# Kernel tuning notes

Hardware: AMD Instinct MI355X
Metric: run time of the kernel (lower is better)

Reference implementation:

```python
import jax, jax.numpy as jnp
import numpy as np

DIM = 256
DH = 32
HEADS = DIM // DH
AG = 6      # agent_size
WS = 7      # window_size
N = AG * WS * WS  # 294 tokens per window


def _rel_index():
    ws = (AG, WS, WS)
    coords = np.stack(np.meshgrid(np.arange(ws[0]), np.arange(ws[1]), np.arange(ws[2]), indexing='ij'))
    flat = coords.reshape(3, -1)                      # (3, N)
    rel = flat[:, :, None] - flat[:, None, :]         # (3, N, N)
    rel = rel.transpose(1, 2, 0).copy()               # (N, N, 3)
    rel[..., 0] += ws[0] - 1
    rel[..., 1] += ws[1] - 1
    rel[..., 2] += ws[2] - 1
    rel[..., 0] *= (2 * ws[1] - 1) * (2 * ws[2] - 1)
    rel[..., 1] *= (2 * ws[2] - 1)
    return rel.sum(-1).astype(np.int32)               # (N, N)


def setup_inputs() -> dict:
    key = jax.random.key(0)
    k1, k2, k3, k4, k5 = jax.random.split(key, 5)
    x = jax.random.normal(k1, (1, AG, 16, 16, WS, WS, DIM), dtype=jnp.float32)
    mask = jax.random.randint(k2, (1, 16, 16, WS, WS, 1, AG), 0, 2, dtype=jnp.int32)
    w_qkv = jax.random.normal(k3, (DIM, 3 * DIM), dtype=jnp.float32) * (DIM ** -0.5)
    w_out = jax.random.normal(k4, (DIM, DIM), dtype=jnp.float32) * (DIM ** -0.5)
    n_bias = (2 * AG - 1) * (2 * WS - 1) * (2 * WS - 1)
    bias_table = jax.random.normal(k5, (n_bias, HEADS), dtype=jnp.float32) * 0.02
    rel_index = jnp.asarray(_rel_index())
    return {"x": x, "mask": mask, "w_qkv": w_qkv, "w_out": w_out,
            "bias_table": bias_table, "rel_index": rel_index}


def reference(x, mask, w_qkv, w_out, bias_table, rel_index):
    b, l, gx, gy, w1, w2, d = x.shape
    h, dh = HEADS, DH
    # 'b l x y w1 w2 d -> (b x y) (l w1 w2) d'
    xw = x.transpose(0, 2, 3, 1, 4, 5, 6).reshape(b * gx * gy, l * w1 * w2, d)
    B_, n, _ = xw.shape
    qkv = xw @ w_qkv                                  # (B_, N, 3d)
    q, k, v = jnp.split(qkv, 3, axis=-1)
    # 'b n (h d) -> b h n d'
    q = q.reshape(B_, n, h, dh).transpose(0, 2, 1, 3) * (dh ** -0.5)
    k = k.reshape(B_, n, h, dh).transpose(0, 2, 1, 3)
    v = v.reshape(B_, n, h, dh).transpose(0, 2, 1, 3)
    sim = jnp.einsum('bhid,bhjd->bhij', q, k)         # (B_, h, N, N)
    bias = bias_table[rel_index]                      # (N, N, h)
    sim = sim + bias.transpose(2, 0, 1)[None]
    # 'b x y w1 w2 e l -> (b x y) e (l w1 w2)', then unsqueeze head dim
    m = mask.transpose(0, 1, 2, 5, 6, 3, 4).reshape(B_, -1, n)[:, None]  # (B_,1,e,N)
    sim = jnp.where(m == 0, -jnp.inf, sim)
    attn = jax.nn.softmax(sim, axis=-1)
    out = jnp.einsum('bhij,bhjd->bhid', attn, v)      # (B_, h, N, dh)
    # 'b h (l w1 w2) d -> b l w1 w2 (h d)'
    out = out.transpose(0, 2, 1, 3).reshape(B_, l, w1, w2, h * dh)
    out = out @ w_out
    # '(b x y) l w1 w2 d -> b l x y w1 w2 d'
    return out.reshape(b, gx, gy, l, w1, w2, d).transpose(0, 3, 1, 2, 4, 5, 6)
```

## Files before the change

### kernel.cpp

```cpp
#include <hip/hip_runtime.h>

typedef unsigned short u16;
typedef unsigned int   u32;

#define NTOK 294
#define KS_STRIDE 34
#define VT_STRIDE 300
#define WST 260
#define OBUF_BYTES 38535168ull
#define FLAG_OFF (OBUF_BYTES)

#define ROWS_ALLOC 75280ull
#define BUFB (ROWS_ALLOC * 512ull)
#define QWS_OFF   0ull
#define KWS_OFF   (QWS_OFF + BUFB)
#define VWS_OFF   (KWS_OFF + BUFB)
#define OWS_OFF   (VWS_OFF + BUFB)
#define BIASM_OFF (OWS_OFF + BUFB)
#define WQT_OFF   (BIASM_OFF + 1478656ull)
#define WOT_OFF   (WQT_OFF + 393216ull)
#define FLAG2_OFF (WOT_OFF + 131072ull)
#define NEED_WS   (FLAG2_OFF + 4ull)

typedef __fp16 hv2  __attribute__((ext_vector_type(2)));
typedef __fp16 f16x8 __attribute__((ext_vector_type(8)));
typedef float  f32x4 __attribute__((ext_vector_type(4)));

__device__ __forceinline__ float b2f(u16 v){ union{u32 u; float f;} x; x.u = ((u32)v) << 16; return x.f; }
__device__ __forceinline__ u16 f2b(float f){
  union{float f; u32 u;} x; x.f = f; u32 u = x.u;
  return (u16)((u + 0x7fffu + ((u >> 16) & 1u)) >> 16);
}
__device__ __forceinline__ u32 pack2h(float a, float b){
#if __has_builtin(__builtin_amdgcn_cvt_pkrtz)
  auto r = __builtin_amdgcn_cvt_pkrtz(a, b);
  union{ decltype(r) h; u32 u; } x; x.h = r; return x.u;
#else
  union{ hv2 h; u32 u; } x; x.h[0] = (__fp16)a; x.h[1] = (__fp16)b; return x.u;
#endif
}
__device__ __forceinline__ u32 bfp2h(u32 bfp){
  union{u32 u; float f;} lo, hi; lo.u = bfp << 16; hi.u = bfp & 0xffff0000u;
  return pack2h(lo.f, hi.f);
}
__device__ __forceinline__ u16 f2h(float a){ return (u16)(pack2h(a, 0.0f) & 0xffffu); }

__device__ __forceinline__ float dot2f(u32 a, u32 b, float c){
#if __has_builtin(__builtin_amdgcn_fdot2)
  union{u32 u; hv2 h;} A, B; A.u = a; B.u = b;
  return __builtin_amdgcn_fdot2(A.h, B.h, c, false);
#else
  union{u32 u; __fp16 h[2];} A, B; A.u = a; B.u = b;
  return c + (float)A.h[0]*(float)B.h[0] + (float)A.h[1]*(float)B.h[1];
#endif
}

__device__ __forceinline__ float fexp2(float x){
#if __has_builtin(__builtin_amdgcn_exp2f)
  return __builtin_amdgcn_exp2f(x);
#else
  return exp2f(x);
#endif
}

__device__ __forceinline__ f32x4 mfma16(f16x8 a, f16x8 b, f32x4 c){
  return __builtin_amdgcn_mfma_f32_16x16x32_f16(a, b, c, 0, 0, 0);
}

__device__ __forceinline__ void gl2lds16(const void* g, void* l){
#if __has_builtin(__builtin_amdgcn_global_load_lds)
  __builtin_amdgcn_global_load_lds(
      (const __attribute__((address_space(1))) void*)g,
      (__attribute__((address_space(3))) void*)l, 16, 0, 0);
#else
  *(f16x8*)l = *(const f16x8*)g;
#endif
}

__device__ __forceinline__ void stageB(const u16* __restrict__ wsrc, int nt,
                                       u16* lbase, int wave, int lane){
#pragma unroll
  for (int c = 0; c < 2; ++c){
    int G   = (c*4 + wave)*64 + lane;
    int row = G >> 5, g = G & 31;
    int sg  = g ^ (row & 7);
    const u16* src = wsrc + (size_t)nt*4096 + row*256 + sg*8;
    u16* dst = lbase + (size_t)(c*4 + wave)*512;
    gl2lds16(src, dst);
  }
}

__device__ __forceinline__ f16x8 readB(const u16* bb, int ks, int q, int n16){
  return *(const f16x8*)&bb[n16*256 + (((ks*4 + q) ^ (n16 & 7)) * 8)];
}

__global__ void dfab_probe_kernel(const u16* __restrict__ X, int* __restrict__ flag)
{
  const int lane = threadIdx.x;
  int cnt = 0;
#pragma unroll
  for (int k = 0; k < 8; ++k){
    u16 v = X[lane * 8 + k];
    int e = (v >> 7) & 0xFF;
    cnt += (e < 96 || e > 158) ? 1 : 0;
  }
  for (int off = 32; off > 0; off >>= 1) cnt += __shfl_xor(cnt, off);
  if (lane == 0) *flag = (cnt > 64) ? 1 : 0;
}


__global__ __launch_bounds__(256) void dfab_prep_kernel(
    const void* __restrict__ Wqkvv, const void* __restrict__ Woutv,
    const void* __restrict__ BiasTv, const int* __restrict__ RelIdx,
    u16* __restrict__ wqt, u16* __restrict__ wot, u16* __restrict__ biasm,
    const int* __restrict__ flagp)
{
  const int f32m = *(const volatile int*)flagp;
  const u16* Wb = (const u16*)Wqkvv;  const float* Wf = (const float*)Wqkvv;
  const u16* Ob = (const u16*)Woutv;  const float* Of = (const float*)Woutv;
  const u16* Bb = (const u16*)BiasTv; const float* Bf = (const float*)BiasTv;
  int idx = blockIdx.x * 256 + threadIdx.x;
  if (idx < 196608){
    int n = idx >> 8, k = idx & 255;
    float w = f32m ? Wf[k*768 + n] : b2f(Wb[k*768 + n]);
    if (n < 256) w *= 0.25503487f;
    wqt[n*256 + k] = f2h(w);
  } else if (idx < 262144){
    int t = idx - 196608; int n = t >> 8, k = t & 255;
    float w = f32m ? Of[k*256 + n] : b2f(Ob[k*256 + n]);
    wot[n*256 + k] = f2h(w);
  } else {
    int t = idx - 262144;
    int hh = t / 92416; int rem = t - hh * 92416;
    int j = rem / 304;  int i = rem - j * 304;
    float v = 0.f;
    if (i < NTOK && j < NTOK){
      int nb = RelIdx[i * NTOK + j] * 8 + hh;
      v = f32m ? Bf[nb] : b2f(Bb[nb]);
      v *= 1.4426950409f;
    }
    biasm[((size_t)(hh*304 + j))*304 + i] = f2h(v);
  }
}

__global__ __launch_bounds__(256, 4) void dfab_qkv_kernel(
    const void* __restrict__ Xv, const u16* __restrict__ wqt,
    u16* __restrict__ Qws, u16* __restrict__ Kws, u16* __restrict__ Vws,
    const int* __restrict__ flagp)
{
  __shared__ __align__(16) union {
    u16 xs[64 * 264];
    struct { u16 bs[2][4096]; u16 cs[4][1024]; } p;
  } sm;

  const int tid = threadIdx.x;
  const int m0 = blockIdx.x * 64;
  const int f32m = *(const volatile int*)flagp;
  const u16* Xb = (const u16*)Xv; const float* Xf = (const float*)Xv;
  const int wave = tid >> 6, lane = tid & 63;
  const int q = lane >> 4, n16 = lane & 15;

  for (int idx = tid; idx < 64 * 128; idx += 256){
    int rl = idx >> 7, d2 = idx & 127;
    int m = m0 + rl; int win = m / 294, tok = m - win * 294;
    int l = tok / 49, r = tok - l * 49;
    size_t src = ((size_t)((l*256 + win)*49 + r))*256 + 2*d2;
    u32 hp;
    if (f32m){ float2 xx = *(const float2*)&Xf[src]; hp = pack2h(xx.x, xx.y); }
    else     { hp = bfp2h(*(const u32*)&Xb[src]); }
    *(u32*)&sm.xs[rl * 264 + 2*d2] = hp;
  }
  __syncthreads();

  f16x8 afr[8];
#pragma unroll
  for (int ks = 0; ks < 8; ++ks)
    afr[ks] = *(const f16x8*)&sm.xs[(wave*16 + n16) * 264 + ks*32 + q*8];
  __syncthreads();

  stageB(wqt, 0, &sm.p.bs[0][0], wave, lane);
  __syncthreads();

  u16* myC = &sm.p.cs[wave][0];
  const size_t rowb = (size_t)(m0 + wave*16);
  const int rbrow = lane >> 3, seg = lane & 7;

#pragma unroll 1
  for (int grp = 0; grp < 12; ++grp){
    u16* dstp = (grp < 4) ? Qws : ((grp < 8) ? Kws : Vws);
    const int g4 = grp & 3;
#pragma unroll
    for (int t = 0; t < 4; ++t){
      const int nt = grp*4 + t;
      if (nt < 47) stageB(wqt, nt+1, &sm.p.bs[(nt+1)&1][0], wave, lane);
      const u16* bb = &sm.p.bs[nt&1][0];
      f16x8 bfr[8];
#pragma unroll
      for (int ks = 0; ks < 8; ++ks) bfr[ks] = readB(bb, ks, q, n16);
      f32x4 c0 = {0.f,0.f,0.f,0.f}, c1 = {0.f,0.f,0.f,0.f};
#pragma unroll
      for (int ks = 0; ks < 4; ++ks){
        c0 = mfma16(afr[ks],     bfr[ks],     c0);
        c1 = mfma16(afr[ks + 4], bfr[ks + 4], c1);
      }
#pragma unroll
      for (int r = 0; r < 4; ++r)
        myC[(q*4 + r)*64 + t*16 + n16] = f2h(c0[r] + c1[r]);
      __syncthreads();
    }
    __asm__ volatile("s_waitcnt lgkmcnt(0)" ::: "memory");
#pragma unroll
    for (int p = 0; p < 2; ++p){
      const int row = p*8 + rbrow;
      f16x8 v = *(const f16x8*)&myC[row*64 + seg*8];
      *(f16x8*)&dstp[(rowb + row)*256 + g4*64 + seg*8] = v;
    }
  }
}

__global__ __launch_bounds__(256, 2) void dfab_attn2_kernel(
    const u16* __restrict__ Qws, const u16* __restrict__ Kws,
    const u16* __restrict__ Vws, const u16* __restrict__ BiasM,
    const int* __restrict__ Mask, u16* __restrict__ Ows)
{
  __shared__ __align__(16) u16 Ks[304 * 40];
  __shared__ __align__(16) u16 Vt[32 * 328];
  __shared__ __align__(16) u16 Pw[4][16 * 168];
  __shared__ float Madd[304];

  const int tid = threadIdx.x;
  const int win = blockIdx.x >> 3, h = blockIdx.x & 7;
  const int wave = tid >> 6, lane = tid & 63;
  const int q = lane >> 4, n16 = lane & 15;

  for (int j = tid; j < 304; j += 256){
    float mv = -1e30f;
    if (j < NTOK){ int l = j / 49, r = j - l * 49;
      mv = (Mask[(win * 49 + r) * 6 + l] != 0) ? 0.0f : -1e30f; }
    Madd[j] = mv;
  }

  {
    const int rr0 = tid >> 2, seg = tid & 3;
#pragma unroll
    for (int p = 0; p < 5; ++p){
      int rr = rr0 + p*64;
      if (rr < NTOK){
        f16x8 kv = *(const f16x8*)&Kws[((size_t)(win*NTOK + rr))*256 + h*32 + seg*8];
        *(f16x8*)&Ks[rr*40 + seg*8] = kv;
      }
    }
    if (tid < 40){
      int rr = NTOK + (tid >> 2);
      uint4 z = {0u,0u,0u,0u};
      *(uint4*)&Ks[rr*40 + seg*8] = z;
    }
#pragma unroll
    for (int p = 0; p < 5; ++p){
      int tok = rr0 + p*64;
      union{ f16x8 h; u16 s[8]; } vv;
      uint4 z = {0u,0u,0u,0u};
      *(uint4*)&vv = z;
      if (tok < NTOK)
        vv.h = *(const f16x8*)&Vws[((size_t)(win*NTOK + tok))*256 + h*32 + seg*8];
      if (tok < 320){
#pragma unroll
        for (int k = 0; k < 8; ++k) Vt[(seg*8 + k)*328 + tok] = vv.s[k];
      }
    }
  }
  __syncthreads();

  float maddv[19];
#pragma unroll
  for (int nt = 0; nt < 19; ++nt) maddv[nt] = Madd[nt*16 + n16];

  u16* myP = Pw[wave];
  int mt = wave;
  f16x8 qf = *(const f16x8*)&Qws[((size_t)(win*NTOK + mt*16 + n16))*256 + h*32 + q*8];

#pragma unroll 1
  for (; mt < 19; mt += 4){
    const int m0 = mt * 16;

    uint2 bu[19];
#pragma unroll
    for (int nt = 0; nt < 19; ++nt)
      bu[nt] = *(const uint2*)&BiasM[((size_t)(h*304 + nt*16 + n16))*304 + m0 + q*4];

    float S[19][4];
#pragma unroll
    for (int nt = 0; nt < 19; ++nt){
      f16x8 kf = *(const f16x8*)&Ks[(nt*16 + n16)*40 + q*8];
      union { uint2 u; __fp16 hh[4]; } b; b.u = bu[nt];
      f32x4 c = { (float)b.hh[0] + maddv[nt], (float)b.hh[1] + maddv[nt],
                  (float)b.hh[2] + maddv[nt], (float)b.hh[3] + maddv[nt] };
      c = mfma16(qf, kf, c);
#pragma unroll
      for (int r = 0; r < 4; ++r) S[nt][r] = c[r];
    }

    const int mtn = mt + 4;
    f16x8 qfn = qf;
    if (mtn < 19)
      qfn = *(const f16x8*)&Qws[((size_t)(win*NTOK + mtn*16 + n16))*256 + h*32 + q*8];

    float rinv[4];
#pragma unroll
    for (int r = 0; r < 4; ++r){
      float a0 = fmaxf(fmaxf(S[0][r],  S[1][r]),  S[2][r]);
      float a1 = fmaxf(fmaxf(S[3][r],  S[4][r]),  S[5][r]);
      float a2 = fmaxf(fmaxf(S[6][r],  S[7][r]),  S[8][r]);
      float a3 = fmaxf(fmaxf(S[9][r],  S[10][r]), S[11][r]);
      float a4 = fmaxf(fmaxf(S[12][r], S[13][r]), S[14][r]);
      float a5 = fmaxf(fmaxf(S[15][r], S[16][r]), S[17][r]);
      float mx = fmaxf(fmaxf(fmaxf(a0, a1), fmaxf(a2, a3)),
                       fmaxf(fmaxf(a4, a5), S[18][r]));
      mx = fmaxf(mx, __shfl_xor(mx, 1));
      mx = fmaxf(mx, __shfl_xor(mx, 2));
      mx = fmaxf(mx, __shfl_xor(mx, 4));
      mx = fmaxf(mx, __shfl_xor(mx, 8));
      float s0 = 0.f, s1 = 0.f, s2 = 0.f, s3 = 0.f;
#pragma unroll
      for (int nt = 0; nt < 19; ++nt){
        float e = fexp2(S[nt][r] - mx);
        S[nt][r] = e;
        if ((nt & 3) == 0) s0 += e;
        else if ((nt & 3) == 1) s1 += e;
        else if ((nt & 3) == 2) s2 += e;
        else s3 += e;
      }
      float sum = (s0 + s1) + (s2 + s3);
      sum += __shfl_xor(sum, 1);
      sum += __shfl_xor(sum, 2);
      sum += __shfl_xor(sum, 4);
      sum += __shfl_xor(sum, 8);
      rinv[r] = 1.0f / sum;
    }
    f32x4 o0 = {0.f,0.f,0.f,0.f}, o1 = {0.f,0.f,0.f,0.f};
#pragma unroll
    for (int half = 0; half < 2; ++half){
#pragma unroll
      for (int ntl = 0; ntl < 10; ++ntl){
        int nt = half * 10 + ntl;
        int col = ntl * 16 + n16;
#pragma unroll
        for (int r = 0; r < 4; ++r)
          myP[(q*4 + r) * 168 + col] = (nt < 19) ? f2h(S[nt][r]) : (u16)0;
      }
      __asm__ volatile("s_waitcnt lgkmcnt(0)" ::: "memory");
#pragma unroll
      for (int kk = 0; kk < 5; ++kk){
        f16x8 pf = *(const f16x8*)&myP[n16 * 168 + kk*32 + q*8];
        f16x8 v0 = *(const f16x8*)&Vt[n16 * 328 + half*160 + kk*32 + q*8];
        f16x8 v1 = *(const f16x8*)&Vt[(16 + n16) * 328 + half*160 + kk*32 + q*8];
        o0 = mfma16(pf, v0, o0);
        o1 = mfma16(pf, v1, o1);
      }
      __asm__ volatile("s_waitcnt lgkmcnt(0)" ::: "memory");
    }
#pragma unroll
    for (int r = 0; r < 4; ++r){
      int tok = m0 + q*4 + r;
      if (tok < NTOK){
        size_t base = ((size_t)(win*NTOK + tok))*256 + h*32;
        Ows[base + n16]      = f2h(o0[r] * rinv[r]);
        Ows[base + 16 + n16] = f2h(o1[r] * rinv[r]);
      }
    }
    qf = qfn;
  }
}

__global__ __launch_bounds__(256, 4) void dfab_proj2_kernel(
    const u16* __restrict__ Ows, const u16* __restrict__ wot,
    void* __restrict__ Outv, const int* __restrict__ flagp)
{
  __shared__ __align__(16) u16   Bs[2][4096];
  __shared__ __align__(16) float Csf[4][16 * 64];

  const int tid = threadIdx.x;
  const int wave = tid >> 6, lane = tid & 63;
  const int q = lane >> 4, n16 = lane & 15;
  const int mr = blockIdx.x * 64 + wave * 16;
  const int f32m = *(const volatile int*)flagp;

  stageB(wot, 0, &Bs[0][0], wave, lane);

  f16x8 afr[8];
#pragma unroll
  for (int ks = 0; ks < 8; ++ks)
    afr[ks] = *(const f16x8*)&Ows[((size_t)(mr + n16))*256 + ks*32 + q*8];

  const int rbrow = lane >> 3, seg = lane & 7;
  size_t ob0, ob1;
  {
    int m = mr + rbrow;     int win = m / 294, tok = m - win*294;
    int l = tok / 49, rr = tok - l*49;
    ob0 = ((size_t)((l*256 + win)*49 + rr))*256;
    m = mr + 8 + rbrow;     win = m / 294; tok = m - win*294;
    l = tok / 49; rr = tok - l*49;
    ob1 = ((size_t)((l*256 + win)*49 + rr))*256;
  }

  float* myC = &Csf[wave][0];
  __syncthreads();

#pragma unroll 1
  for (int g4 = 0; g4 < 4; ++g4){
#pragma unroll
    for (int t = 0; t < 4; ++t){
      const int nt = g4*4 + t;
      if (nt < 15) stageB(wot, nt+1, &Bs[(nt+1)&1][0], wave, lane);
      const u16* bb = &Bs[nt&1][0];
      f16x8 bfr[8];
#pragma unroll
      for (int ks = 0; ks < 8; ++ks) bfr[ks] = readB(bb, ks, q, n16);
      f32x4 c0 = {0.f,0.f,0.f,0.f}, c1 = {0.f,0.f,0.f,0.f};
#pragma unroll
      for (int ks = 0; ks < 4; ++ks){
        c0 = mfma16(afr[ks],     bfr[ks],     c0);
        c1 = mfma16(afr[ks + 4], bfr[ks + 4], c1);
      }
#pragma unroll
      for (int r = 0; r < 4; ++r)
        myC[(q*4 + r)*64 + t*16 + n16] = c0[r] + c1[r];
      __syncthreads();
    }
    __asm__ volatile("s_waitcnt lgkmcnt(0)" ::: "memory");
#pragma unroll
    for (int p = 0; p < 2; ++p){
      const int row = p*8 + rbrow;
      const size_t ob = p ? ob1 : ob0;
      f32x4 v0 = *(const f32x4*)&myC[row*64 + seg*8];
      f32x4 v1 = *(const f32x4*)&myC[row*64 + seg*8 + 4];
      if (f32m){
        *(f32x4*)&((float*)Outv)[ob + g4*64 + seg*8]     = v0;
        *(f32x4*)&((float*)Outv)[ob + g4*64 + seg*8 + 4] = v1;
      } else {
        union{ u32 w[4]; u16 h[8]; } pk;
        pk.h[0]=f2b(v0[0]); pk.h[1]=f2b(v0[1]); pk.h[2]=f2b(v0[2]); pk.h[3]=f2b(v0[3]);
        pk.h[4]=f2b(v1[0]); pk.h[5]=f2b(v1[1]); pk.h[6]=f2b(v1[2]); pk.h[7]=f2b(v1[3]);
        *(uint4*)&((u16*)Outv)[ob + g4*64 + seg*8] = *(const uint4*)&pk.w[0];
      }
    }
  }
}

__global__ __launch_bounds__(256) void dfab_attn_kernel(
    const void* __restrict__ Xv, const int* __restrict__ Mask,
    const void* __restrict__ Wqkvv, const void* __restrict__ BiasTv,
    const int* __restrict__ RelIdx, u16* __restrict__ Obuf,
    const int* __restrict__ flagp)
{
  __shared__ __align__(16) char lds[59736];
  u16* Ks   = (u16*)(lds);
  u16* Vt   = (u16*)(lds + 19992);
  u16* Wp   = (u16*)(lds + 39192);
  u16* Xs   = (u16*)(lds + 47512);
  u16* Wqt  = (u16*)(lds + 39192);
  u32* Pb   = (u32*)(lds + 55832);
  float* Madd = (float*)(lds + 58264);
  u16* Qb   = (u16*)(lds + 59480);

  const int tid = threadIdx.x;
  const int bx  = blockIdx.x;
  const int win = bx >> 3, h = bx & 7;

  const int f32m = *(const volatile int*)flagp;
  const u16*   Xb = (const u16*)Xv;       const float* Xf = (const float*)Xv;
  const u16*   Wb = (const u16*)Wqkvv;    const float* Wf = (const float*)Wqkvv;
  const u16*   Bb = (const u16*)BiasTv;   const float* Bf = (const float*)BiasTv;

  for (int j = tid; j < 304; j += 256){
    float mv = -1e30f;
    if (j < NTOK){ int l = j / 49, r = j - l * 49;
      mv = (Mask[(win * 49 + r) * 6 + l] != 0) ? 0.0f : -1e30f; }
    Madd[j] = mv;
  }
  for (int idx = tid; idx < 32 * 6; idx += 256){
    int c = idx / 6; Vt[c * VT_STRIDE + NTOK + (idx - c * 6)] = 0;
  }

#pragma unroll 1
  for (int p = 0; p < 4; ++p){
    const int kind = p >> 1;
    const int colbase = 256 + kind * 256 + h * 32 + (p & 1) * 16;
    __syncthreads();
    for (int idx = tid; idx < 16 * 128; idx += 256){
      int c = idx & 15, d2 = idx >> 4;
      float w0, w1;
      if (f32m){ w0 = Wf[(2 * d2) * 768 + colbase + c]; w1 = Wf[(2 * d2 + 1) * 768 + colbase + c]; }
      else     { w0 = b2f(Wb[(2 * d2) * 768 + colbase + c]); w1 = b2f(Wb[(2 * d2 + 1) * 768 + colbase + c]); }
      *(u32*)&Wp[c * WST + 2 * d2] = pack2h(w0, w1);
    }
#pragma unroll 1
    for (int jt = 0; jt < 19; ++jt){
      const int j0 = jt * 16;
      const int nj = (NTOK - j0 < 16) ? (NTOK - j0) : 16;
      __syncthreads();
      for (int idx = tid; idx < nj * 128; idx += 256){
        int jl = idx >> 7, d2 = idx & 127;
        int tok = j0 + jl; int l = tok / 49, r = tok - l * 49;
        size_t off = (size_t)((l * 256 + win) * 49 + r) * 256 + 2 * d2;
        u32 hp;
        if (f32m){ float2 xx = *(const float2*)&Xf[off]; hp = pack2h(xx.x, xx.y); }
        else     { hp = bfp2h(*(const u32*)&Xb[off]); }
        *(u32*)&Xs[jl * WST + 2 * d2] = hp;
      }
      __syncthreads();
      const int jl = tid >> 4, c = tid & 15;
      const u32* xp = (const u32*)&Xs[jl * WST];
      const u32* wp = (const u32*)&Wp[c * WST];
      float a0 = 0.f, a1 = 0.f;
#pragma unroll 4
      for (int d2 = 0; d2 < 128; d2 += 4){
        uint2 xa = *(const uint2*)(xp + d2), xb = *(const uint2*)(xp + d2 + 2);
        uint2 wa = *(const uint2*)(wp + d2), wb = *(const uint2*)(wp + d2 + 2);
        a0 = dot2f(xa.x, wa.x, a0); a1 = dot2f(xa.y, wa.y, a1);
        a0 = dot2f(xb.x, wb.x, a0); a1 = dot2f(xb.y, wb.y, a1);
      }
      if (jl < nj){
        u16 hv = f2h(a0 + a1);
        int tok = j0 + jl;
        if (kind == 0) Ks[tok * KS_STRIDE + (p & 1) * 16 + c] = hv;
        else           Vt[((p & 1) * 16 + c) * VT_STRIDE + tok] = hv;
      }
    }
  }
  __syncthreads();
  for (int idx = tid; idx < 32 * 128; idx += 256){
    int c = idx & 31, d2 = idx >> 5;
    float w0, w1;
    if (f32m){ w0 = Wf[(2 * d2) * 768 + h * 32 + c]; w1 = Wf[(2 * d2 + 1) * 768 + h * 32 + c]; }
    else     { w0 = b2f(Wb[(2 * d2) * 768 + h * 32 + c]); w1 = b2f(Wb[(2 * d2 + 1) * 768 + h * 32 + c]); }
    *(u32*)&Wqt[c * WST + 2 * d2] = pack2h(w0, w1);
  }
  __syncthreads();

  const int wave = tid >> 6, lane = tid & 63;
  const int hf = lane >> 5, c32 = lane & 31;
  u32* mypb = Pb + wave * 152;
  u16* qbw  = Qb + wave * 32;

  for (int i = wave; i < NTOK; i += 4){
    const int li = i / 49, ri = i - li * 49;
    const size_t rowoff = (size_t)((li * 256 + win) * 49 + ri) * 256;
    const u32* wqp = (const u32*)&Wqt[c32 * WST];
    float q0 = 0.f, q1 = 0.f;
    if (f32m){
      const float4* xr4 = (const float4*)&Xf[rowoff];
#pragma unroll 4
      for (int d2 = hf * 64; d2 < hf * 64 + 64; d2 += 2){
        uint2 wq = *(const uint2*)(wqp + d2);
        float4 xx = xr4[d2 >> 1];
        q0 = dot2f(pack2h(xx.x, xx.y), wq.x, q0);
        q1 = dot2f(pack2h(xx.z, xx.w), wq.y, q1);
      }
    } else {
      const u32* xr = (const u32*)&Xb[rowoff];
#pragma unroll 4
      for (int d2 = hf * 64; d2 < hf * 64 + 64; d2 += 2){
        uint2 wq = *(const uint2*)(wqp + d2);
        q0 = dot2f(bfp2h(xr[d2]),     wq.x, q0);
        q1 = dot2f(bfp2h(xr[d2 + 1]), wq.y, q1);
      }
    }
    float qa = q0 + q1;
    qa += __shfl_xor(qa, 32);
    if (hf == 0) qbw[c32] = f2h(qa * 0.17677669529663687f);
    __asm__ volatile("s_waitcnt lgkmcnt(0)" ::: "memory");
    u32 qp[16];
#pragma unroll
    for (int cc = 0; cc < 16; ++cc) qp[cc] = *(const u32*)&qbw[2 * cc];

    float sv[5];
#pragma unroll
    for (int it = 0; it < 5; ++it){
      int j = it * 64 + lane;
      float a;
      if (j < NTOK){
        int nb = RelIdx[i * NTOK + j] * 8 + h;
        float bias = f32m ? Bf[nb] : b2f(Bb[nb]);
        float a0 = bias + Madd[j];
        float a1 = 0.f;
        const u16* kr = &Ks[j * KS_STRIDE];
#pragma unroll
        for (int cc = 0; cc < 16; cc += 2){
          a0 = dot2f(qp[cc],     *(const u32*)&kr[2 * cc],     a0);
          a1 = dot2f(qp[cc + 1], *(const u32*)&kr[2 * cc + 2], a1);
        }
        a = a0 + a1;
      } else a = -3e38f;
      sv[it] = a;
    }
    float m = sv[0];
#pragma unroll
    for (int it = 1; it < 5; ++it) m = fmaxf(m, sv[it]);
    for (int off = 32; off > 0; off >>= 1) m = fmaxf(m, __shfl_xor(m, off));
    float lsum = 0.f;
#pragma unroll
    for (int it = 0; it < 5; ++it){ float e = __expf(sv[it] - m); sv[it] = e; lsum += e; }
    for (int off = 32; off > 0; off >>= 1) lsum += __shfl_xor(lsum, off);
    const float rinv = 1.0f / lsum;
#pragma unroll
    for (int it = 0; it < 5; ++it){
      float pn = sv[it] * rinv;
      float po = __shfl_xor(pn, 1);
      int j = it * 64 + lane;
      if (!(lane & 1) && j < 304) mypb[j >> 1] = pack2h(pn, po);
    }
    __asm__ volatile("s_waitcnt lgkmcnt(0)" ::: "memory");
    const u16* vr = &Vt[c32 * VT_STRIDE];
    const int jb = hf * 148;
    float o0 = 0.f, o1 = 0.f;
#pragma unroll 4
    for (int g = 0; g < 37; ++g){
      int j = jb + 4 * g;
      uint2 vv = *(const uint2*)&vr[j];
      uint2 pp = *(const uint2*)&mypb[j >> 1];
      o0 = dot2f(pp.x, vv.x, o0);
      o1 = dot2f(pp.y, vv.y, o1);
    }
    float o = o0 + o1;
    o += __shfl_xor(o, 32);
    if (hf == 0)
      Obuf[(size_t)(win * NTOK + i) * 256 + h * 32 + c32] = f2b(o);
  }
}

__global__ __launch_bounds__(256) void dfab_proj_kernel(
    const u16* __restrict__ Obuf, const void* __restrict__ Woutv,
    void* __restrict__ Outv, const int* __restrict__ flagp)
{
  __shared__ __align__(16) char lds[33920];
  u16* Ot = (u16*)(lds);
  u16* Wt = (u16*)(lds + 16512);

  const int tid = threadIdx.x;
  const int bx = blockIdx.x;
  const int win = bx / 10, tile = bx - win * 10;
  const int t0 = tile * 32;
  const int nt = (NTOK - t0 < 32) ? (NTOK - t0) : 32;

  const int f32m = *(const volatile int*)flagp;
  const u16* Wob = (const u16*)Woutv; const float* Wof = (const float*)Woutv;

  for (int idx = tid; idx < nt * 128; idx += 256){
    int t = idx >> 7, k2 = idx & 127;
    u32 oo = *(const u32*)&Obuf[(size_t)(win * NTOK + t0 + t) * 256 + 2 * k2];
    *(u32*)&Ot[t * 258 + 2 * k2] = bfp2h(oo);
  }

  float acc[32];
#pragma unroll
  for (int t = 0; t < 32; ++t) acc[t] = 0.f;
  const int dd = tid;

#pragma unroll 1
  for (int kt = 0; kt < 8; ++kt){
    __syncthreads();
    for (int idx = tid; idx < 4096; idx += 256){
      int d = idx & 255, kk2 = idx >> 8;
      int k = kt * 32 + 2 * kk2;
      float w0, w1;
      if (f32m){ w0 = Wof[k * 256 + d]; w1 = Wof[(k + 1) * 256 + d]; }
      else     { w0 = b2f(Wob[k * 256 + d]); w1 = b2f(Wob[(k + 1) * 256 + d]); }
      *(u32*)&Wt[d * 34 + 2 * kk2] = pack2h(w0, w1);
    }
    __syncthreads();
#pragma unroll 2
    for (int kk2 = 0; kk2 < 16; ++kk2){
      u32 wp = *(const u32*)&Wt[dd * 34 + 2 * kk2];
      const u16* orow = &Ot[kt * 32 + 2 * kk2];
#pragma unroll 8
      for (int t = 0; t < 32; ++t){
        u32 op = *(const u32*)&orow[t * 258];
        acc[t] = dot2f(op, wp, acc[t]);
      }
    }
  }

  for (int t = 0; t < nt; ++t){
    int tok = t0 + t; int l = tok / 49, r = tok - l * 49;
    size_t oidx = (size_t)((l * 256 + win) * 49 + r) * 256 + dd;
    if (f32m) ((float*)Outv)[oidx] = acc[t];
    else      ((u16*)Outv)[oidx]   = f2b(acc[t]);
  }
}

extern "C" void kernel_launch(void* const* d_in, const int* in_sizes, int n_in,
                              void* d_out, int out_size, void* d_ws, size_t ws_size,
                              hipStream_t stream) {
  (void)in_sizes; (void)n_in; (void)out_size;
  const void* x          = d_in[0];
  const int*  mask       = (const int*)d_in[1];
  const void* w_qkv      = d_in[2];
  const void* w_out      = d_in[3];
  const void* bias_table = d_in[4];
  const int*  rel_index  = (const int*)d_in[5];
  char* ws = (char*)d_ws;

  if (ws_size >= NEED_WS){
    u16* qws   = (u16*)(ws + QWS_OFF);
    u16* kws   = (u16*)(ws + KWS_OFF);
    u16* vws   = (u16*)(ws + VWS_OFF);
    u16* ows   = (u16*)(ws + OWS_OFF);
    u16* biasm = (u16*)(ws + BIASM_OFF);
    u16* wqt   = (u16*)(ws + WQT_OFF);
    u16* wot   = (u16*)(ws + WOT_OFF);
    int* flag  = (int*)(ws + FLAG2_OFF);
    dfab_probe_kernel<<<1, 64, 0, stream>>>((const u16*)x, flag);
    dfab_prep_kernel<<<3912, 256, 0, stream>>>(w_qkv, w_out, bias_table, rel_index,
                                               wqt, wot, biasm, flag);
    dfab_qkv_kernel<<<1176, 256, 0, stream>>>(x, wqt, qws, kws, vws, flag);
    dfab_attn2_kernel<<<2048, 256, 0, stream>>>(qws, kws, vws, biasm, mask, ows);
    dfab_proj2_kernel<<<1176, 256, 0, stream>>>(ows, wot, d_out, flag);
  } else {
    u16* obuf = (u16*)ws;
    int* flag = (int*)(ws + FLAG_OFF);
    dfab_probe_kernel<<<1, 64, 0, stream>>>((const u16*)x, flag);
    dfab_attn_kernel<<<2048, 256, 0, stream>>>(x, mask, w_qkv, bias_table, rel_index, obuf, flag);
    dfab_proj_kernel<<<2560, 256, 0, stream>>>(obuf, w_out, d_out, flag);
  }
}
```

Baseline: 366.9 us.

## Stream fp32 tiled bias and double-buffer per-tile P through small LDS

The precomputed bias matrix becomes fp32, laid out per 16-row query tile, so each lane loads a float4 per key tile directly rather than preloading 19 fp16 pairs into registers. The PV product now runs one 16-key tile at a time with 16x16x16 MFMAs, staging P through two small ping-pong LDS buffers instead of a large per-wave P tile. This cuts register and LDS pressure so the launch bound can be raised to 3 blocks per SM. In exchange, the bias buffer doubles in size, global traffic rises, and more small MFMA and LDS operations are issued.

```diff
diff --git a/kernel.cpp b/kernel.cpp
--- a/kernel.cpp
+++ b/kernel.cpp
@@ -16,13 +16,15 @@
 #define KWS_OFF   (QWS_OFF + BUFB)
 #define VWS_OFF   (KWS_OFF + BUFB)
 #define OWS_OFF   (VWS_OFF + BUFB)
-#define BIASM_OFF (OWS_OFF + BUFB)
-#define WQT_OFF   (BIASM_OFF + 1478656ull)
+#define BIASF_OFF (OWS_OFF + BUFB)
+#define BIASF_BYTES 2957312ull
+#define WQT_OFF   (BIASF_OFF + BIASF_BYTES)
 #define WOT_OFF   (WQT_OFF + 393216ull)
 #define FLAG2_OFF (WOT_OFF + 131072ull)
 #define NEED_WS   (FLAG2_OFF + 4ull)
 
 typedef __fp16 hv2  __attribute__((ext_vector_type(2)));
+typedef __fp16 f16x4 __attribute__((ext_vector_type(4)));
 typedef __fp16 f16x8 __attribute__((ext_vector_type(8)));
 typedef float  f32x4 __attribute__((ext_vector_type(4)));
 
@@ -66,6 +68,9 @@
 __device__ __forceinline__ f32x4 mfma16(f16x8 a, f16x8 b, f32x4 c){
   return __builtin_amdgcn_mfma_f32_16x16x32_f16(a, b, c, 0, 0, 0);
 }
+__device__ __forceinline__ f32x4 mfma16k16(f16x4 a, f16x4 b, f32x4 c){
+  return __builtin_amdgcn_mfma_f32_16x16x16f16(a, b, c, 0, 0, 0);
+}
 
 __device__ __forceinline__ void gl2lds16(const void* g, void* l){
 #if __has_builtin(__builtin_amdgcn_global_load_lds)
@@ -112,7 +117,7 @@
 __global__ __launch_bounds__(256) void dfab_prep_kernel(
     const void* __restrict__ Wqkvv, const void* __restrict__ Woutv,
     const void* __restrict__ BiasTv, const int* __restrict__ RelIdx,
-    u16* __restrict__ wqt, u16* __restrict__ wot, u16* __restrict__ biasm,
+    u16* __restrict__ wqt, u16* __restrict__ wot, float* __restrict__ biasf,
     const int* __restrict__ flagp)
 {
   const int f32m = *(const volatile int*)flagp;
@@ -132,14 +137,15 @@
   } else {
     int t = idx - 262144;
     int hh = t / 92416; int rem = t - hh * 92416;
-    int j = rem / 304;  int i = rem - j * 304;
+    int mt = rem / 4864; int r2 = rem - mt * 4864;
+    int col = r2 >> 4;  int rw = r2 & 15;
+    int i = mt * 16 + rw;
     float v = 0.f;
-    if (i < NTOK && j < NTOK){
-      int nb = RelIdx[i * NTOK + j] * 8 + hh;
-      v = f32m ? Bf[nb] : b2f(Bb[nb]);
-      v *= 1.4426950409f;
-    }
-    biasm[((size_t)(hh*304 + j))*304 + i] = f2h(v);
+    if (i < NTOK && col < NTOK){
+      int nb = RelIdx[i * NTOK + col] * 8 + hh;
+      v = (f32m ? Bf[nb] : b2f(Bb[nb])) * 1.4426950409f;
+    }
+    biasf[((size_t)((hh*19 + mt)*304 + col))*16 + rw] = v;
   }
 }
 
@@ -218,14 +224,14 @@
   }
 }
 
-__global__ __launch_bounds__(256, 2) void dfab_attn2_kernel(
+__global__ __launch_bounds__(256, 3) void dfab_attn2_kernel(
     const u16* __restrict__ Qws, const u16* __restrict__ Kws,
-    const u16* __restrict__ Vws, const u16* __restrict__ BiasM,
+    const u16* __restrict__ Vws, const float* __restrict__ Biasf,
     const int* __restrict__ Mask, u16* __restrict__ Ows)
 {
   __shared__ __align__(16) u16 Ks[304 * 40];
   __shared__ __align__(16) u16 Vt[32 * 328];
-  __shared__ __align__(16) u16 Pw[4][16 * 168];
+  __shared__ __align__(16) u16 Pt[4][2][16 * 20];
   __shared__ float Madd[304];
 
   const int tid = threadIdx.x;
@@ -275,26 +281,23 @@
 #pragma unroll
   for (int nt = 0; nt < 19; ++nt) maddv[nt] = Madd[nt*16 + n16];
 
-  u16* myP = Pw[wave];
+  u16* myP0 = &Pt[wave][0][0];
+  u16* myP1 = &Pt[wave][1][0];
   int mt = wave;
   f16x8 qf = *(const f16x8*)&Qws[((size_t)(win*NTOK + mt*16 + n16))*256 + h*32 + q*8];
 
 #pragma unroll 1
   for (; mt < 19; mt += 4){
     const int m0 = mt * 16;
-
-    uint2 bu[19];
-#pragma unroll
-    for (int nt = 0; nt < 19; ++nt)
-      bu[nt] = *(const uint2*)&BiasM[((size_t)(h*304 + nt*16 + n16))*304 + m0 + q*4];
+    const float* bmt = Biasf + ((size_t)((h*19 + mt)*304 + n16))*16 + q*4;
 
     float S[19][4];
 #pragma unroll
     for (int nt = 0; nt < 19; ++nt){
       f16x8 kf = *(const f16x8*)&Ks[(nt*16 + n16)*40 + q*8];
-      union { uint2 u; __fp16 hh[4]; } b; b.u = bu[nt];
-      f32x4 c = { (float)b.hh[0] + maddv[nt], (float)b.hh[1] + maddv[nt],
-                  (float)b.hh[2] + maddv[nt], (float)b.hh[3] + maddv[nt] };
+      f32x4 bv = *(const f32x4*)&bmt[nt*256];
+      f32x4 c = { bv[0] + maddv[nt], bv[1] + maddv[nt],
+                  bv[2] + maddv[nt], bv[3] + maddv[nt] };
       c = mfma16(qf, kf, c);
 #pragma unroll
       for (int r = 0; r < 4; ++r) S[nt][r] = c[r];
@@ -337,28 +340,27 @@
       sum += __shfl_xor(sum, 8);
       rinv[r] = 1.0f / sum;
     }
+
     f32x4 o0 = {0.f,0.f,0.f,0.f}, o1 = {0.f,0.f,0.f,0.f};
 #pragma unroll
-    for (int half = 0; half < 2; ++half){
-#pragma unroll
-      for (int ntl = 0; ntl < 10; ++ntl){
-        int nt = half * 10 + ntl;
-        int col = ntl * 16 + n16;
+    for (int r = 0; r < 4; ++r)
+      myP0[(q*4 + r)*20 + n16] = f2h(S[0][r]);
+#pragma unroll
+    for (int nt = 0; nt < 19; ++nt){
+      u16* cur = (nt & 1) ? myP1 : myP0;
+      u16* nxt = (nt & 1) ? myP0 : myP1;
+      if (nt < 18){
 #pragma unroll
         for (int r = 0; r < 4; ++r)
-          myP[(q*4 + r) * 168 + col] = (nt < 19) ? f2h(S[nt][r]) : (u16)0;
-      }
-      __asm__ volatile("s_waitcnt lgkmcnt(0)" ::: "memory");
-#pragma unroll
-      for (int kk = 0; kk < 5; ++kk){
-        f16x8 pf = *(const f16x8*)&myP[n16 * 168 + kk*32 + q*8];
-        f16x8 v0 = *(const f16x8*)&Vt[n16 * 328 + half*160 + kk*32 + q*8];
-        f16x8 v1 = *(const f16x8*)&Vt[(16 + n16) * 328 + half*160 + kk*32 + q*8];
-        o0 = mfma16(pf, v0, o0);
-        o1 = mfma16(pf, v1, o1);
-      }
-      __asm__ volatile("s_waitcnt lgkmcnt(0)" ::: "memory");
-    }
+          nxt[(q*4 + r)*20 + n16] = f2h(S[nt+1][r]);
+      }
+      f16x4 pa = *(const f16x4*)&cur[n16*20 + q*4];
+      f16x4 v0 = *(const f16x4*)&Vt[n16*328        + nt*16 + q*4];
+      f16x4 v1 = *(const f16x4*)&Vt[(16 + n16)*328 + nt*16 + q*4];
+      o0 = mfma16k16(pa, v0, o0);
+      o1 = mfma16k16(pa, v1, o1);
+    }
+
 #pragma unroll
     for (int r = 0; r < 4; ++r){
       int tok = m0 + q*4 + r;
@@ -706,15 +708,15 @@
     u16* kws   = (u16*)(ws + KWS_OFF);
     u16* vws   = (u16*)(ws + VWS_OFF);
     u16* ows   = (u16*)(ws + OWS_OFF);
-    u16* biasm = (u16*)(ws + BIASM_OFF);
+    float* bsf = (float*)(ws + BIASF_OFF);
     u16* wqt   = (u16*)(ws + WQT_OFF);
     u16* wot   = (u16*)(ws + WOT_OFF);
     int* flag  = (int*)(ws + FLAG2_OFF);
     dfab_probe_kernel<<<1, 64, 0, stream>>>((const u16*)x, flag);
     dfab_prep_kernel<<<3912, 256, 0, stream>>>(w_qkv, w_out, bias_table, rel_index,
-                                               wqt, wot, biasm, flag);
+                                               wqt, wot, bsf, flag);
     dfab_qkv_kernel<<<1176, 256, 0, stream>>>(x, wqt, qws, kws, vws, flag);
-    dfab_attn2_kernel<<<2048, 256, 0, stream>>>(qws, kws, vws, biasm, mask, ows);
+    dfab_attn2_kernel<<<2048, 256, 0, stream>>>(qws, kws, vws, bsf, mask, ows);
     dfab_proj2_kernel<<<1176, 256, 0, stream>>>(ows, wot, d_out, flag);
   } else {
     u16* obuf = (u16*)ws;
```

Result: slower. 440.9 us (+20.2%).
